# Optimization experiments

Hardware: AMD Instinct MI355X
Metric: run time of the kernel (lower is better)

## Reference

```python
import jax, jax.numpy as jnp
import numpy as np
import math

B, S, E, H = 4, 2048, 1024, 16
D = E // H
NEG_INF = -1e30  # stands in for -inf in masked_fill; softmax result identical for rows with valid entries


def setup_inputs() -> dict:
    key = jax.random.key(0)
    ks = jax.random.split(key, 7)
    sc = 1.0 / math.sqrt(E)
    return {
        "k": jax.random.normal(ks[0], (B, S, E), jnp.float32),
        "v": jax.random.normal(ks[1], (B, S, E), jnp.float32),
        "q": jax.random.normal(ks[2], (B, S, E), jnp.float32),
        "Wk": jax.random.normal(ks[3], (E, E), jnp.float32) * sc,
        "Wv": jax.random.normal(ks[4], (E, E), jnp.float32) * sc,
        "Wq": jax.random.normal(ks[5], (E, E), jnp.float32) * sc,
        "Wo": jax.random.normal(ks[6], (E, E), jnp.float32) * sc,
    }


def reference(k, v, q, Wk, Wv, Wq, Wo):
    # Linear(bias=False): y = x @ W.T
    kp = (k @ Wk.T).reshape(B, S, H, D).transpose(0, 2, 1, 3)  # [B,H,S,D]
    vp = (v @ Wv.T).reshape(B, S, H, D).transpose(0, 2, 1, 3)
    qp = (q @ Wq.T).reshape(B, S, H, D).transpose(0, 2, 1, 3)
    qp = qp / jnp.sqrt(jnp.asarray(D, qp.dtype))
    scores = jnp.einsum("bhqd,bhkd->bhqk", qp, kp)  # [B,H,S,S]
    causal = jnp.tril(jnp.ones((S, S), bool))  # [S,S]
    scores = jnp.where(causal[None, None], scores, NEG_INF)
    attn = jax.nn.softmax(scores, axis=-1)  # dropout p=0.0 (eval) -> identity
    out = jnp.einsum("bhqk,bhkd->bhqd", attn, vp)
    out = out.transpose(0, 2, 1, 3).reshape(B, S, E)
    return out @ Wo.T
```

## Files before the change

### kernel.cpp

```cpp
#include <hip/hip_runtime.h>

typedef __bf16 bf16_t;
typedef __bf16 bf16x8 __attribute__((ext_vector_type(8)));
typedef float f32x4 __attribute__((ext_vector_type(4)));
typedef float f32x16 __attribute__((ext_vector_type(16)));


__device__ __forceinline__ void async_copy16(const void* g, void* l) {
  __builtin_amdgcn_global_load_lds(
      (const __attribute__((address_space(1))) void*)g,
      (__attribute__((address_space(3))) void*)l, 16, 0, 0);
}

__device__ __forceinline__ unsigned pk_bf16(float lo, float hi) {
  unsigned r;
  asm("v_cvt_pk_bf16_f32 %0, %1, %2" : "=v"(r) : "v"(lo), "v"(hi));
  return r;
}

__global__ void cvt_all_kernel(const float* __restrict__ q, const float* __restrict__ k,
                               const float* __restrict__ v, const float* __restrict__ wk,
                               const float* __restrict__ wv, const float* __restrict__ wq,
                               const float* __restrict__ wo, uint2* __restrict__ out) {
  constexpr int QX = 2097152, QW = 262144;
  int g = blockIdx.x * 256 + threadIdx.x;
  const float* in; int off;
  if (g < QX)               { in = q;  off = 0; }
  else if (g < 2 * QX)      { in = k;  off = QX; }
  else if (g < 3 * QX)      { in = v;  off = 2 * QX; }
  else if (g < 3 * QX + QW)     { in = wk; off = 3 * QX; }
  else if (g < 3 * QX + 2 * QW) { in = wv; off = 3 * QX + QW; }
  else if (g < 3 * QX + 3 * QW) { in = wq; off = 3 * QX + 2 * QW; }
  else                          { in = wo; off = 3 * QX + 3 * QW; }
  float4 val = ((const float4*)in)[g - off];
  union { bf16_t h[4]; uint2 u; } cv;
  cv.h[0] = (bf16_t)val.x; cv.h[1] = (bf16_t)val.y;
  cv.h[2] = (bf16_t)val.z; cv.h[3] = (bf16_t)val.w;
  out[g] = cv.u;
}

__global__ __launch_bounds__(256) void qkv_kernel(
    const bf16_t* __restrict__ qb, const bf16_t* __restrict__ kb, const bf16_t* __restrict__ vb,
    const bf16_t* __restrict__ wqb, const bf16_t* __restrict__ wkb, const bf16_t* __restrict__ wvb,
    bf16_t* __restrict__ Qp, bf16_t* __restrict__ Kp, bf16_t* __restrict__ Vt, float qscale)
{
  constexpr int K = 1024;
  __shared__ __align__(16) bf16_t As[128 * 32];
  __shared__ __align__(16) bf16_t Bs[128 * 32];
  const int tid  = threadIdx.x;
  const int lane = tid & 63;
  const int wid  = tid >> 6;
  const int quad = lane >> 4;
  const int l16  = lane & 15;
  const int bx = blockIdx.x, by = blockIdx.y;
  const int sel = by >> 3, sub = by & 7;
  const bf16_t *X, *W; bf16_t* Y; float scale = 1.0f;
  int m0, n0;
  if (sel == 0)      { X = qb;  W = wqb; Y = Qp; m0 = bx * 128; n0 = sub * 128; scale = qscale; }
  else if (sel == 1) { X = kb;  W = wkb; Y = Kp; m0 = bx * 128; n0 = sub * 128; }
  else               { X = wvb; W = vb;  Y = Vt; m0 = sub * 128; n0 = bx * 128; }
  const int wm = (wid >> 1) * 64;
  const int wn = (wid & 1) * 64;
  const int swz = quad ^ ((l16 >> 1) & 3);

  f32x4 acc[4][4] = {};

  for (int k0 = 0; k0 < K; k0 += 32) {
#pragma unroll
    for (int p = 0; p < 2; ++p) {
      int c = tid + p * 256;
      int row = c >> 2;
      int seg = ((c & 3) ^ ((c >> 3) & 3)) * 8;
      async_copy16(&X[(size_t)(m0 + row) * K + k0 + seg], (char*)As + (p * 256 + wid * 64) * 16);
      async_copy16(&W[(size_t)(n0 + row) * K + k0 + seg], (char*)Bs + (p * 256 + wid * 64) * 16);
    }
    __syncthreads();
    bf16x8 af[4], bfr[4];
#pragma unroll
    for (int i = 0; i < 4; ++i)
      af[i] = *(const bf16x8*)((const char*)As + ((wm + i * 16 + l16) * 4 + swz) * 16);
#pragma unroll
    for (int j = 0; j < 4; ++j)
      bfr[j] = *(const bf16x8*)((const char*)Bs + ((wn + j * 16 + l16) * 4 + swz) * 16);
#pragma unroll
    for (int i = 0; i < 4; ++i)
#pragma unroll
      for (int j = 0; j < 4; ++j)
        acc[i][j] = __builtin_amdgcn_mfma_f32_16x16x32_bf16(af[i], bfr[j], acc[i][j], 0, 0, 0);
    __syncthreads();
  }

#pragma unroll
  for (int i = 0; i < 4; ++i)
#pragma unroll
    for (int j = 0; j < 4; ++j)
#pragma unroll
      for (int r = 0; r < 4; ++r) {
        int row = m0 + wm + i * 16 + quad * 4 + r;
        int col = n0 + wn + j * 16 + l16;
        float val = acc[i][j][r] * scale;
        if (sel < 2) {
          int b = row >> 11, s = row & 2047;
          int h = col >> 6,  d = col & 63;
          Y[(((size_t)(b * 16 + h) << 11) + s) * 64 + d] = (bf16_t)val;
        } else {
          int h = row >> 6,  d = row & 63;
          int b = col >> 11, s = col & 2047;
          Y[(((size_t)((b * 16 + h) * 64 + d)) << 11) + s] = (bf16_t)val;
        }
      }
}

__global__ __launch_bounds__(256) void out_gemm_kernel(
    const bf16_t* __restrict__ X, const bf16_t* __restrict__ W,
    float* __restrict__ Y, int M, int N, int K)
{
  __shared__ __align__(16) bf16_t As[128 * 32];
  __shared__ __align__(16) bf16_t Bs[128 * 32];
  const int tid  = threadIdx.x;
  const int lane = tid & 63;
  const int wid  = tid >> 6;
  const int quad = lane >> 4;
  const int l16  = lane & 15;
  const int m0 = blockIdx.x * 128;
  const int n0 = blockIdx.y * 128;
  const int wm = (wid >> 1) * 64;
  const int wn = (wid & 1) * 64;
  const int swz = quad ^ ((l16 >> 1) & 3);

  f32x4 acc[4][4] = {};

  for (int k0 = 0; k0 < K; k0 += 32) {
#pragma unroll
    for (int p = 0; p < 2; ++p) {
      int c = tid + p * 256;
      int row = c >> 2;
      int seg = ((c & 3) ^ ((c >> 3) & 3)) * 8;
      async_copy16(&X[(size_t)(m0 + row) * K + k0 + seg], (char*)As + (p * 256 + wid * 64) * 16);
      async_copy16(&W[(size_t)(n0 + row) * K + k0 + seg], (char*)Bs + (p * 256 + wid * 64) * 16);
    }
    __syncthreads();
    bf16x8 af[4], bfr[4];
#pragma unroll
    for (int i = 0; i < 4; ++i)
      af[i] = *(const bf16x8*)((const char*)As + ((wm + i * 16 + l16) * 4 + swz) * 16);
#pragma unroll
    for (int j = 0; j < 4; ++j)
      bfr[j] = *(const bf16x8*)((const char*)Bs + ((wn + j * 16 + l16) * 4 + swz) * 16);
#pragma unroll
    for (int i = 0; i < 4; ++i)
#pragma unroll
      for (int j = 0; j < 4; ++j)
        acc[i][j] = __builtin_amdgcn_mfma_f32_16x16x32_bf16(af[i], bfr[j], acc[i][j], 0, 0, 0);
    __syncthreads();
  }

#pragma unroll
  for (int i = 0; i < 4; ++i)
#pragma unroll
    for (int j = 0; j < 4; ++j)
#pragma unroll
      for (int r = 0; r < 4; ++r) {
        int row = m0 + wm + i * 16 + quad * 4 + r;
        int col = n0 + wn + j * 16 + l16;
        Y[(size_t)row * N + col] = acc[i][j][r];
      }
}

__global__ __launch_bounds__(256, 3) void attn_kernel(
    const bf16_t* __restrict__ Qp, const bf16_t* __restrict__ Kp,
    const bf16_t* __restrict__ Vt, bf16_t* __restrict__ O)
{
  constexpr int S = 2048, D = 64, E = 1024;
  constexpr int BQ = 128, BK = 64;
  __shared__ __align__(16) bf16_t Ks[2][8 * 64 * 8];
  __shared__ __align__(16) bf16_t Vs[2][8 * 64 * 8];
  __shared__ float rsbuf[128];

  const int tid = threadIdx.x, lane = tid & 63, wid = tid >> 6;
  const int l31 = lane & 31, hi = lane >> 5;
  const int bh = blockIdx.y;
  const int b = bh >> 4, h = bh & 15;
  const int qt = (int)gridDim.x - 1 - (int)blockIdx.x;
  const int q0 = qt * BQ;
  const size_t base  = (size_t)bh * S * D;
  const size_t baseV = (size_t)bh * D * S;
  const int qmin = q0 + wid * 32;
  const int qmax = qmin + 31;

  bf16x8 qf[4];
#pragma unroll
  for (int ks = 0; ks < 4; ++ks)
    qf[ks] = *(const bf16x8*)&Qp[base + (size_t)(qmin + l31) * D + ks * 16 + hi * 8];

#pragma unroll
  for (int is = 0; is < 2; ++is) {
    const int c = is * 256 + tid;
    const int p = c >> 6, row = c & 63;
    async_copy16(&Kp[base + (size_t)row * D + p * 8],
                 (char*)Ks[0] + (is * 256 + wid * 64) * 16);
    async_copy16(&Vt[baseV + (size_t)row * S + p * 8],
                 (char*)Vs[0] + (is * 256 + wid * 64) * 16);
  }
  __syncthreads();

  const f32x16 z16 = {};
  f32x16 oa0 = {}, oa1 = {};
  float rs = 0.0f;
  const int nks = 2 * qt + 2;

  for (int kt = 0; kt < nks; ++kt) {
    const int cur = kt & 1;
    const int k0 = kt * BK;
    if (kt + 1 < nks) {
      const int k0n = k0 + BK;
#pragma unroll
      for (int is = 0; is < 2; ++is) {
        const int c = is * 256 + tid;
        const int p = c >> 6, row = c & 63;
        async_copy16(&Kp[base + (size_t)(k0n + row) * D + p * 8],
                     (char*)Ks[cur ^ 1] + (is * 256 + wid * 64) * 16);
        async_copy16(&Vt[baseV + (size_t)row * S + k0n + p * 8],
                     (char*)Vs[cur ^ 1] + (is * 256 + wid * 64) * 16);
      }
    }
    if (k0 <= qmax) {
      const bf16_t* ksb = Ks[cur];
      const bf16_t* vsb = Vs[cur];
      f32x16 sc0, sc1;
      {
        const bf16x8 kf0 = *(const bf16x8*)&ksb[(hi * 64 + l31) * 8];
        const bf16x8 kf1 = *(const bf16x8*)&ksb[(hi * 64 + 32 + l31) * 8];
        sc0 = __builtin_amdgcn_mfma_f32_32x32x16_bf16(kf0, qf[0], z16, 0, 0, 0);
        sc1 = __builtin_amdgcn_mfma_f32_32x32x16_bf16(kf1, qf[0], z16, 0, 0, 0);
      }
#pragma unroll
      for (int ks = 1; ks < 4; ++ks) {
        const bf16x8 kf0 = *(const bf16x8*)&ksb[((ks * 2 + hi) * 64 + l31) * 8];
        const bf16x8 kf1 = *(const bf16x8*)&ksb[((ks * 2 + hi) * 64 + 32 + l31) * 8];
        sc0 = __builtin_amdgcn_mfma_f32_32x32x16_bf16(kf0, qf[ks], sc0, 0, 0, 0);
        sc1 = __builtin_amdgcn_mfma_f32_32x32x16_bf16(kf1, qf[ks], sc1, 0, 0, 0);
      }
      if (k0 + 63 > qmin) {
        const int qg = qmin + l31;
#pragma unroll
        for (int r = 0; r < 16; ++r) {
          const int kg = k0 + (r & 3) + 8 * (r >> 2) + 4 * hi;
          if (kg > qg)      sc0[r] = -1e30f;
          if (kg + 32 > qg) sc1[r] = -1e30f;
        }
      }
#pragma unroll
      for (int r = 0; r < 16; ++r) {
        sc0[r] = __builtin_amdgcn_exp2f(sc0[r]);
        sc1[r] = __builtin_amdgcn_exp2f(sc1[r]);
      }
      {
        float s0 = 0.f, s1 = 0.f, s2 = 0.f, s3 = 0.f;
#pragma unroll
        for (int r = 0; r < 16; r += 4) {
          s0 += sc0[r]     + sc1[r];
          s1 += sc0[r + 1] + sc1[r + 1];
          s2 += sc0[r + 2] + sc1[r + 2];
          s3 += sc0[r + 3] + sc1[r + 3];
        }
        rs += (s0 + s1) + (s2 + s3);
      }
      unsigned pw[16];
      {
        unsigned a0 = pk_bf16(sc0[0], sc0[1]),   a1 = pk_bf16(sc0[2], sc0[3]);
        unsigned b0 = pk_bf16(sc0[4], sc0[5]),   b1 = pk_bf16(sc0[6], sc0[7]);
        unsigned c0 = pk_bf16(sc0[8], sc0[9]),   c1 = pk_bf16(sc0[10], sc0[11]);
        unsigned d0 = pk_bf16(sc0[12], sc0[13]), d1 = pk_bf16(sc0[14], sc0[15]);
        asm("v_permlane32_swap_b32 %0, %1" : "+v"(a0), "+v"(b0));
        asm("v_permlane32_swap_b32 %0, %1" : "+v"(a1), "+v"(b1));
        asm("v_permlane32_swap_b32 %0, %1" : "+v"(c0), "+v"(d0));
        asm("v_permlane32_swap_b32 %0, %1" : "+v"(c1), "+v"(d1));
        pw[0] = a0; pw[1] = a1; pw[2] = b0; pw[3] = b1;
        pw[4] = c0; pw[5] = c1; pw[6] = d0; pw[7] = d1;
      }
      {
        unsigned a0 = pk_bf16(sc1[0], sc1[1]),   a1 = pk_bf16(sc1[2], sc1[3]);
        unsigned b0 = pk_bf16(sc1[4], sc1[5]),   b1 = pk_bf16(sc1[6], sc1[7]);
        unsigned c0 = pk_bf16(sc1[8], sc1[9]),   c1 = pk_bf16(sc1[10], sc1[11]);
        unsigned d0 = pk_bf16(sc1[12], sc1[13]), d1 = pk_bf16(sc1[14], sc1[15]);
        asm("v_permlane32_swap_b32 %0, %1" : "+v"(a0), "+v"(b0));
        asm("v_permlane32_swap_b32 %0, %1" : "+v"(a1), "+v"(b1));
        asm("v_permlane32_swap_b32 %0, %1" : "+v"(c0), "+v"(d0));
        asm("v_permlane32_swap_b32 %0, %1" : "+v"(c1), "+v"(d1));
        pw[8]  = a0; pw[9]  = a1; pw[10] = b0; pw[11] = b1;
        pw[12] = c0; pw[13] = c1; pw[14] = d0; pw[15] = d1;
      }
      union U8 { unsigned u[4]; bf16x8 v; };
#pragma unroll
      for (int kb = 0; kb < 2; ++kb)
#pragma unroll
        for (int ks2 = 0; ks2 < 2; ++ks2) {
          U8 pu;
          pu.u[0] = pw[kb * 8 + ks2 * 4 + 0];
          pu.u[1] = pw[kb * 8 + ks2 * 4 + 1];
          pu.u[2] = pw[kb * 8 + ks2 * 4 + 2];
          pu.u[3] = pw[kb * 8 + ks2 * 4 + 3];
          const int pnl = kb * 4 + ks2 * 2 + hi;
          const bf16x8 vf0 = *(const bf16x8*)&vsb[(pnl * 64 + l31) * 8];
          const bf16x8 vf1 = *(const bf16x8*)&vsb[(pnl * 64 + 32 + l31) * 8];
          oa0 = __builtin_amdgcn_mfma_f32_32x32x16_bf16(pu.v, vf0, oa0, 0, 0, 0);
          oa1 = __builtin_amdgcn_mfma_f32_32x32x16_bf16(pu.v, vf1, oa1, 0, 0, 0);
        }
    }
    __syncthreads();
  }

  const float full = rs + __shfl(rs, lane ^ 32);
  if (lane < 32) rsbuf[wid * 32 + l31] = full;
  __syncthreads();
#pragma unroll
  for (int r = 0; r < 16; ++r) {
    const int crow = (r & 3) + 8 * (r >> 2) + 4 * hi;
    const float inv = __builtin_amdgcn_rcpf(rsbuf[wid * 32 + crow]);
    const int row = q0 + wid * 32 + crow;
    const size_t rowoff = ((size_t)(b * S + row)) * E + h * D;
    O[rowoff + l31]      = (bf16_t)(oa0[r] * inv);
    O[rowoff + 32 + l31] = (bf16_t)(oa1[r] * inv);
  }
}

extern "C" void kernel_launch(void* const* d_in, const int* in_sizes, int n_in,
                              void* d_out, int out_size, void* d_ws, size_t ws_size,
                              hipStream_t stream) {
  const float* k_in = (const float*)d_in[0];
  const float* v_in = (const float*)d_in[1];
  const float* q_in = (const float*)d_in[2];
  const float* Wk_in = (const float*)d_in[3];
  const float* Wv_in = (const float*)d_in[4];
  const float* Wq_in = (const float*)d_in[5];
  const float* Wo_in = (const float*)d_in[6];
  float* out = (float*)d_out;

  constexpr int    M = 8192, N = 1024, K = 1024;
  constexpr size_t SZ_X = (size_t)M * K * 2;
  constexpr size_t SZ_W = (size_t)N * K * 2;

  char* ws = (char*)d_ws;
  bf16_t* qb  = (bf16_t*)(ws);
  bf16_t* kb  = (bf16_t*)(ws + SZ_X);
  bf16_t* vb  = (bf16_t*)(ws + 2 * SZ_X);
  bf16_t* wkb = (bf16_t*)(ws + 3 * SZ_X);
  bf16_t* wvb = (bf16_t*)(ws + 3 * SZ_X + SZ_W);
  bf16_t* wqb = (bf16_t*)(ws + 3 * SZ_X + 2 * SZ_W);
  bf16_t* wob = (bf16_t*)(ws + 3 * SZ_X + 3 * SZ_W);
  bf16_t* Qp  = (bf16_t*)(ws + 3 * SZ_X + 4 * SZ_W);
  bf16_t* Kp  = (bf16_t*)(ws + 4 * SZ_X + 4 * SZ_W);
  bf16_t* Vtg = (bf16_t*)(ws + 5 * SZ_X + 4 * SZ_W);
  bf16_t* Ob  = qb;

  cvt_all_kernel<<<28672, 256, 0, stream>>>(q_in, k_in, v_in, Wk_in, Wv_in, Wq_in, Wo_in,
                                            (uint2*)ws);

  qkv_kernel<<<dim3(64, 24), 256, 0, stream>>>(qb, kb, vb, wqb, wkb, wvb,
                                               Qp, Kp, Vtg, 0.125f * 1.44269504f);

  attn_kernel<<<dim3(2048 / 128, 4 * 16), 256, 0, stream>>>(Qp, Kp, Vtg, Ob);

  out_gemm_kernel<<<dim3(M / 128, N / 128), 256, 0, stream>>>(Ob, wob, out, M, N, K);
}
```

Before: 323.4 us.

## Split long causal query tiles across two blocks and reduce partials

The eight longest causal query tiles (the upper half of the sequence) now have their key range split between two blocks. Each block writes an unnormalized fp32 partial output and row sum to workspace, and a new normalization kernel adds the two halves and writes bf16. The aim is to even out per-block work and cut the tail of the causal triangle. In exchange it adds fp32 partial traffic through global memory and an extra kernel launch, and it reuses workspace regions whose inputs are already consumed.

```diff
diff --git a/kernel.cpp b/kernel.cpp
--- a/kernel.cpp
+++ b/kernel.cpp
@@ -169,7 +169,8 @@
 
 __global__ __launch_bounds__(256, 3) void attn_kernel(
     const bf16_t* __restrict__ Qp, const bf16_t* __restrict__ Kp,
-    const bf16_t* __restrict__ Vt, bf16_t* __restrict__ O)
+    const bf16_t* __restrict__ Vt, bf16_t* __restrict__ O,
+    float* __restrict__ Oacc, float* __restrict__ Racc)
 {
   constexpr int S = 2048, D = 64, E = 1024;
   constexpr int BQ = 128, BK = 64;
@@ -181,7 +182,22 @@
   const int l31 = lane & 31, hi = lane >> 5;
   const int bh = blockIdx.y;
   const int b = bh >> 4, h = bh & 15;
-  const int qt = (int)gridDim.x - 1 - (int)blockIdx.x;
+
+  const int bx = blockIdx.x;
+  int qt, s0, s1, half; bool direct;
+  if (bx < 16) {
+    qt = 15 - (bx >> 1);
+    const int nks = 2 * qt + 2;
+    half = bx & 1;
+    s0 = half ? nks / 2 : 0;
+    s1 = half ? nks : nks / 2;
+    direct = false;
+  } else {
+    qt = 23 - bx;
+    s0 = 0; s1 = 2 * qt + 2; half = 0;
+    direct = true;
+  }
+
   const int q0 = qt * BQ;
   const size_t base  = (size_t)bh * S * D;
   const size_t baseV = (size_t)bh * D * S;
@@ -193,26 +209,28 @@
   for (int ks = 0; ks < 4; ++ks)
     qf[ks] = *(const bf16x8*)&Qp[base + (size_t)(qmin + l31) * D + ks * 16 + hi * 8];
 
-#pragma unroll
-  for (int is = 0; is < 2; ++is) {
-    const int c = is * 256 + tid;
-    const int p = c >> 6, row = c & 63;
-    async_copy16(&Kp[base + (size_t)row * D + p * 8],
-                 (char*)Ks[0] + (is * 256 + wid * 64) * 16);
-    async_copy16(&Vt[baseV + (size_t)row * S + p * 8],
-                 (char*)Vs[0] + (is * 256 + wid * 64) * 16);
+  {
+    const int kb0 = s0 * BK;
+#pragma unroll
+    for (int is = 0; is < 2; ++is) {
+      const int c = is * 256 + tid;
+      const int p = c >> 6, row = c & 63;
+      async_copy16(&Kp[base + (size_t)(kb0 + row) * D + p * 8],
+                   (char*)Ks[s0 & 1] + (is * 256 + wid * 64) * 16);
+      async_copy16(&Vt[baseV + (size_t)row * S + kb0 + p * 8],
+                   (char*)Vs[s0 & 1] + (is * 256 + wid * 64) * 16);
+    }
   }
   __syncthreads();
 
   const f32x16 z16 = {};
   f32x16 oa0 = {}, oa1 = {};
   float rs = 0.0f;
-  const int nks = 2 * qt + 2;
-
-  for (int kt = 0; kt < nks; ++kt) {
+
+  for (int kt = s0; kt < s1; ++kt) {
     const int cur = kt & 1;
     const int k0 = kt * BK;
-    if (kt + 1 < nks) {
+    if (kt + 1 < s1) {
       const int k0n = k0 + BK;
 #pragma unroll
       for (int is = 0; is < 2; ++is) {
@@ -256,15 +274,15 @@
         sc1[r] = __builtin_amdgcn_exp2f(sc1[r]);
       }
       {
-        float s0 = 0.f, s1 = 0.f, s2 = 0.f, s3 = 0.f;
+        float s0a = 0.f, s1a = 0.f, s2a = 0.f, s3a = 0.f;
 #pragma unroll
         for (int r = 0; r < 16; r += 4) {
-          s0 += sc0[r]     + sc1[r];
-          s1 += sc0[r + 1] + sc1[r + 1];
-          s2 += sc0[r + 2] + sc1[r + 2];
-          s3 += sc0[r + 3] + sc1[r + 3];
+          s0a += sc0[r]     + sc1[r];
+          s1a += sc0[r + 1] + sc1[r + 1];
+          s2a += sc0[r + 2] + sc1[r + 2];
+          s3a += sc0[r + 3] + sc1[r + 3];
         }
-        rs += (s0 + s1) + (s2 + s3);
+        rs += (s0a + s1a) + (s2a + s3a);
       }
       unsigned pw[16];
       {
@@ -312,17 +330,53 @@
   }
 
   const float full = rs + __shfl(rs, lane ^ 32);
-  if (lane < 32) rsbuf[wid * 32 + l31] = full;
-  __syncthreads();
-#pragma unroll
-  for (int r = 0; r < 16; ++r) {
-    const int crow = (r & 3) + 8 * (r >> 2) + 4 * hi;
-    const float inv = __builtin_amdgcn_rcpf(rsbuf[wid * 32 + crow]);
-    const int row = q0 + wid * 32 + crow;
-    const size_t rowoff = ((size_t)(b * S + row)) * E + h * D;
-    O[rowoff + l31]      = (bf16_t)(oa0[r] * inv);
-    O[rowoff + 32 + l31] = (bf16_t)(oa1[r] * inv);
-  }
+  if (direct) {
+    if (lane < 32) rsbuf[wid * 32 + l31] = full;
+    __syncthreads();
+#pragma unroll
+    for (int r = 0; r < 16; ++r) {
+      const int crow = (r & 3) + 8 * (r >> 2) + 4 * hi;
+      const float inv = __builtin_amdgcn_rcpf(rsbuf[wid * 32 + crow]);
+      const int row = q0 + wid * 32 + crow;
+      const size_t rowoff = ((size_t)(b * S + row)) * E + h * D;
+      O[rowoff + l31]      = (bf16_t)(oa0[r] * inv);
+      O[rowoff + 32 + l31] = (bf16_t)(oa1[r] * inv);
+    }
+  } else {
+    float* Oh = Oacc + (size_t)half * (64 * 1024 * 64);
+    float* Rh = Racc + (size_t)half * (64 * 1024);
+    if (lane < 32) Rh[(size_t)bh * 1024 + (qmin + l31 - 1024)] = full;
+#pragma unroll
+    for (int r = 0; r < 16; ++r) {
+      const int crow = (r & 3) + 8 * (r >> 2) + 4 * hi;
+      const int row = q0 + wid * 32 + crow;
+      float* dst = &Oh[((size_t)bh * 1024 + (row - 1024)) * 64];
+      dst[l31]      = oa0[r];
+      dst[32 + l31] = oa1[r];
+    }
+  }
+}
+
+__global__ void attn_norm_kernel(const float* __restrict__ Oacc,
+                                 const float* __restrict__ Racc,
+                                 bf16_t* __restrict__ O) {
+  constexpr size_t OHALF = (size_t)64 * 1024 * 64;
+  constexpr size_t RHALF = (size_t)64 * 1024;
+  const int g = blockIdx.x * 256 + threadIdx.x;
+  const int r = g >> 4;
+  const int dq = (g & 15) * 4;
+  const int bh = r >> 10, srow = r & 1023;
+  const int b = bh >> 4, h = bh & 15;
+  const float4 v0 = *(const float4*)&Oacc[(size_t)r * 64 + dq];
+  const float4 v1 = *(const float4*)&Oacc[OHALF + (size_t)r * 64 + dq];
+  const float inv = __builtin_amdgcn_rcpf(Racc[r] + Racc[RHALF + r]);
+  union { bf16_t hh[4]; uint2 u; } cv;
+  cv.hh[0] = (bf16_t)((v0.x + v1.x) * inv);
+  cv.hh[1] = (bf16_t)((v0.y + v1.y) * inv);
+  cv.hh[2] = (bf16_t)((v0.z + v1.z) * inv);
+  cv.hh[3] = (bf16_t)((v0.w + v1.w) * inv);
+  const size_t off = ((size_t)(b * 2048 + 1024 + srow)) * 1024 + h * 64 + dq;
+  *(uint2*)&O[off] = cv.u;
 }
 
 extern "C" void kernel_launch(void* const* d_in, const int* in_sizes, int n_in,
@@ -353,6 +407,8 @@
   bf16_t* Kp  = (bf16_t*)(ws + 4 * SZ_X + 4 * SZ_W);
   bf16_t* Vtg = (bf16_t*)(ws + 5 * SZ_X + 4 * SZ_W);
   bf16_t* Ob  = qb;
+  float* Oacc = (float*)(ws + SZ_X);
+  float* Racc = (float*)(ws + 3 * SZ_X);
 
   cvt_all_kernel<<<28672, 256, 0, stream>>>(q_in, k_in, v_in, Wk_in, Wv_in, Wq_in, Wo_in,
                                             (uint2*)ws);
@@ -360,7 +416,9 @@
   qkv_kernel<<<dim3(64, 24), 256, 0, stream>>>(qb, kb, vb, wqb, wkb, wvb,
                                                Qp, Kp, Vtg, 0.125f * 1.44269504f);
 
-  attn_kernel<<<dim3(2048 / 128, 4 * 16), 256, 0, stream>>>(Qp, Kp, Vtg, Ob);
+  attn_kernel<<<dim3(24, 4 * 16), 256, 0, stream>>>(Qp, Kp, Vtg, Ob, Oacc, Racc);
+
+  attn_norm_kernel<<<4096, 256, 0, stream>>>(Oacc, Racc, Ob);
 
   out_gemm_kernel<<<dim3(M / 128, N / 128), 256, 0, stream>>>(Ob, wob, out, M, N, K);
 }
```

New measurement: 325.4 us. No clear change (+0.6%).
